# Kernel tuning notes

Hardware: AMD Instinct MI355X
Metric: run time of the kernel (lower is better)

## Reference

```python
import jax, jax.numpy as jnp
import numpy as np

N = 20000        # atoms
NEIGH = 12       # neighbors per atom
BSTEPS = 40      # bond GBF steps, range [0, 8]
ASTEPS = 20      # angle GBF steps, range [-1, 1]
H = 64           # hidden size
NCLS = 2         # n_classification
NCRYS = 20       # crystals (contiguous blocks of 1000 atoms)
NREL = 3         # edge relation types


def gbf(data, dmin, dmax, steps):
    # Gaussian basis expansion: exp(-(d - mu)^2 / gamma^2), gamma = (max-min)/steps
    filters = jnp.linspace(dmin, dmax, steps)
    gamma = (dmax - dmin) / steps
    return jnp.exp(-((data[..., None] - filters) ** 2) / gamma ** 2)


def rgcn(x, src, dst, etype, W_rel, W_root, b):
    # RGCNConv (PyG default): out = x @ W_root + b + sum_r mean_{j in N_r(i)} x_j @ W_r
    out = x @ W_root + b
    for r in range(NREL):
        w = (etype == r).astype(x.dtype)                     # [E]
        msg = (x @ W_rel[r])[src] * w[:, None]               # transform-then-gather: [E, H]
        s = jax.ops.segment_sum(msg, dst, num_segments=x.shape[0])
        c = jax.ops.segment_sum(w, dst, num_segments=x.shape[0])
        out = out + s / jnp.maximum(c, 1.0)[:, None]
    return out


def _forward(bond_fea, angle_fea, species, nbr_idx, crys_idx,
             W1b_rel, W1b_root, b1b, W1a_rel, W1a_root, b1a,
             W2b_rel, W2b_root, b2b, W2a_rel, W2a_root, b2a,
             fc_W, fc_b):
    n = bond_fea.shape[0]
    src = jnp.repeat(jnp.arange(n, dtype=jnp.int32), NEIGH)  # edge sources
    dst = nbr_idx.reshape(-1)                                # edge targets
    etype = species[src] + species[dst]                      # 0/1/2 per species pair

    edge_fea = gbf(bond_fea, 0.0, 8.0, BSTEPS).reshape(n, -1)      # [N, 480]
    ang_fea = gbf(angle_fea, -1.0, 1.0, ASTEPS).reshape(n, -1)     # [N, 2880]

    bf = jax.nn.relu(rgcn(edge_fea, src, dst, etype, W1b_rel, W1b_root, b1b))
    af = jax.nn.relu(rgcn(ang_fea, src, dst, etype, W1a_rel, W1a_root, b1a))
    # dropout treated as identity (eval/deterministic reference)
    bf = jax.nn.relu(rgcn(bf, src, dst, etype, W2b_rel, W2b_root, b2b))
    af = jax.nn.relu(rgcn(af, src, dst, etype, W2a_rel, W2a_root, b2a))

    feat = jnp.concatenate([bf, af], axis=1)                 # [N, 128]

    # pool: mean over contiguous [start, end) ranges per crystal
    starts = crys_idx[:, 0]
    crys_id = jnp.searchsorted(starts, jnp.arange(n), side='right') - 1
    sums = jax.ops.segment_sum(feat, crys_id, num_segments=NCRYS)
    counts = (crys_idx[:, 1] - crys_idx[:, 0]).astype(feat.dtype)[:, None]
    pooled = sums / counts                                   # [NCRYS, 128]

    return pooled @ fc_W + fc_b                              # [NCRYS, NCLS]


def setup_inputs() -> dict:
    key = jax.random.key(0)
    ks = jax.random.split(key, 20)
    bond_fea = jax.random.uniform(ks[0], (N, NEIGH), dtype=jnp.float32) * 8.0
    angle_fea = jax.random.uniform(ks[1], (N, NEIGH, NEIGH), dtype=jnp.float32) * 2.0 - 1.0
    species = jax.random.randint(ks[2], (N,), 0, 2, dtype=jnp.int32)
    nbr_idx = jax.random.randint(ks[3], (N, NEIGH), 0, N, dtype=jnp.int32)
    starts = jnp.arange(NCRYS, dtype=jnp.int32) * (N // NCRYS)
    crys_idx = jnp.stack([starts, starts + (N // NCRYS)], axis=1)

    def w(k, shape, fan_in):
        return jax.random.normal(k, shape, dtype=jnp.float32) / np.sqrt(fan_in)

    in_b = BSTEPS * NEIGH            # 480
    in_a = ASTEPS * NEIGH * NEIGH    # 2880
    return {
        'bond_fea': bond_fea, 'angle_fea': angle_fea, 'species': species,
        'nbr_idx': nbr_idx, 'crys_idx': crys_idx,
        'W1b_rel': w(ks[4], (NREL, in_b, H), in_b), 'W1b_root': w(ks[5], (in_b, H), in_b),
        'b1b': jnp.zeros((H,), jnp.float32),
        'W1a_rel': w(ks[6], (NREL, in_a, H), in_a), 'W1a_root': w(ks[7], (in_a, H), in_a),
        'b1a': jnp.zeros((H,), jnp.float32),
        'W2b_rel': w(ks[8], (NREL, H, H), H), 'W2b_root': w(ks[9], (H, H), H),
        'b2b': jnp.zeros((H,), jnp.float32),
        'W2a_rel': w(ks[10], (NREL, H, H), H), 'W2a_root': w(ks[11], (H, H), H),
        'b2a': jnp.zeros((H,), jnp.float32),
        'fc_W': w(ks[12], (2 * H, NCLS), 2 * H), 'fc_b': jnp.zeros((NCLS,), jnp.float32),
    }


def reference(bond_fea, angle_fea, species, nbr_idx, crys_idx,
              W1b_rel, W1b_root, b1b, W1a_rel, W1a_root, b1a,
              W2b_rel, W2b_root, b2b, W2a_rel, W2a_root, b2a,
              fc_W, fc_b):
    return _forward(bond_fea, angle_fea, species, nbr_idx, crys_idx,
                    W1b_rel, W1b_root, b1b, W1a_rel, W1a_root, b1a,
                    W2b_rel, W2b_root, b2b, W2a_rel, W2a_root, b2a,
                    fc_W, fc_b)
```

## Files before the change

kernel.cpp:

```cpp
#include <hip/hip_runtime.h>

#define NN 20000
#define NNP 20096
#define NEIGH 12
#define NCRYS 20
#define MT2 1256
#define NSUB 16

typedef __bf16 bf16x8 __attribute__((ext_vector_type(8)));
typedef __bf16 bf16x4 __attribute__((ext_vector_type(4)));
typedef float f32x4 __attribute__((ext_vector_type(4)));

__device__ __forceinline__ void pack_one(const float* Wrel, const float* Wroot,
                                         __bf16* Wp, int K, int idx) {
    int k = idx >> 8, n = idx & 255;
    int r = n >> 6, h = n & 63;
    float v = (r < 3) ? Wrel[((size_t)r * K + k) * 64 + h] : Wroot[(size_t)k * 64 + h];
    int kt = k >> 5, k8 = (k >> 3) & 3, j = k & 7, nt = n >> 4, ni = n & 15;
    Wp[((((size_t)kt * 16 + nt) * 4 + k8) * 16 + ni) * 8 + j] = (__bf16)v;
}

__global__ __launch_bounds__(256) void setup_kernel(
    const int* __restrict__ species, const int* __restrict__ nbr,
    int* __restrict__ adj, int* __restrict__ deg,
    const float* __restrict__ W1b_rel, const float* __restrict__ W1b_root,
    const float* __restrict__ W1a_rel, const float* __restrict__ W1a_root,
    const float* __restrict__ W2b_rel, const float* __restrict__ W2b_root,
    const float* __restrict__ W2a_rel, const float* __restrict__ W2a_root,
    __bf16* __restrict__ Wp1b, __bf16* __restrict__ Wp1a,
    __bf16* __restrict__ Wp2b, __bf16* __restrict__ Wp2a,
    const float* __restrict__ bond, const float* __restrict__ angle,
    float* __restrict__ bondT, float* __restrict__ angleT) {
    __shared__ float ls[64 * 145];
    const int bx = blockIdx.x, tid = threadIdx.x;
    if (bx < 938) {
        int e = bx * 256 + tid;
        if (e < NN * NEIGH) {
            int i = e / NEIGH;
            int d = nbr[e];
            int r = species[i] + species[d];
            int slot = atomicAdd(&deg[d], 1);
            if (slot < 64) adj[(size_t)d * 64 + slot] = i | (r << 28);
        }
    } else if (bx < 938 + 256) {
        const int S0 = 480 * 256, S1 = S0 + 2880 * 256, S2 = S1 + 64 * 256, S3 = S2 + 64 * 256;
        for (int idx = (bx - 938) * 256 + tid; idx < S3; idx += 256 * 256) {
            if (idx < S0)       pack_one(W1b_rel, W1b_root, Wp1b, 480, idx);
            else if (idx < S1)  pack_one(W1a_rel, W1a_root, Wp1a, 2880, idx - S0);
            else if (idx < S2)  pack_one(W2b_rel, W2b_root, Wp2b, 64, idx - S1);
            else                pack_one(W2a_rel, W2a_root, Wp2a, 64, idx - S2);
        }
    } else {
        int tb = bx - 1194;
        if (tb < 314) {
            int m0 = tb * 64;
            for (int idx = tid; idx < 64 * 144; idx += 256) {
                int mm = idx / 144, j = idx - mm * 144;
                int m = m0 + mm;
                ls[mm * 145 + j] = (m < NN) ? angle[(size_t)m * 144 + j] : 0.f;
            }
            __syncthreads();
            for (int idx = tid; idx < 144 * 64; idx += 256) {
                int j = idx >> 6, mm = idx & 63;
                angleT[(size_t)j * NNP + m0 + mm] = ls[mm * 145 + j];
            }
        } else {
            int m0 = (tb - 314) * 64;
            for (int idx = tid; idx < 64 * 12; idx += 256) {
                int mm = idx / 12, j = idx - mm * 12;
                int m = m0 + mm;
                ls[mm * 13 + j] = (m < NN) ? bond[(size_t)m * 12 + j] : 0.f;
            }
            __syncthreads();
            for (int idx = tid; idx < 12 * 64; idx += 256) {
                int j = idx >> 6, mm = idx & 63;
                bondT[(size_t)j * NNP + m0 + mm] = ls[mm * 13 + j];
            }
        }
    }
}

template <int MODE>
__device__ __forceinline__ void gemm1_body(const float* __restrict__ xT,
                                           const __bf16* __restrict__ Wp,
                                           float* __restrict__ Y, int mb,
                                           __bf16* __restrict__ Al) {
    constexpr int KTOT = (MODE == 0) ? 480 : 2880;
    constexpr int NKT = KTOT / 32;
    constexpr int DIVN = (MODE == 0) ? 40 : 20;
    constexpr float F0 = (MODE == 0) ? 0.f : -1.f;
    constexpr float FS = (MODE == 0) ? (8.f / 39.f) : (2.f / 19.f);
    constexpr float NG2 = ((MODE == 0) ? -25.f : -100.f) * 1.44269504f;
    const float C  = __builtin_amdgcn_exp2f(2.f * NG2 * FS * FS);
    const float P1 = NG2 * FS * FS;
    const float P2 = -2.f * NG2 * FS;

    const int tid = threadIdx.x;
    const int lane = tid & 63, wv = tid >> 6;
    const int m0 = mb * 64;
    const int smt = tid >> 7;
    const int sk8 = (tid >> 5) & 3;
    const int smi = (tid >> 1) & 15;
    const int sjh = (tid & 1) * 4;
    const int sgm = m0 + smt * 16 + smi;
    const int kk0 = sk8 * 8 + sjh;
    const int swoff = (((smt * 4 + sk8) * 16 + smi) * 8 + sjh);
    const int k8b = lane >> 4, nib = lane & 15;
    const bf16x8* Bg = (const bf16x8*)Wp;

    f32x4 acc[4][2] = {};
    bf16x8 bcur[2], bnx[2], bnx2[2];

    auto bload = [&](int kt, bf16x8* d) {
#pragma unroll
        for (int jf = 0; jf < 2; ++jf)
            d[jf] = Bg[(((size_t)kt * 16 + 2 * wv + jf) * 4 + k8b) * 16 + nib];
    };
    auto aload = [&](int kt) -> float {
        int k = kt * 32 + kk0;
        int jr = k / DIVN;
        return xT[(size_t)jr * NNP + sgm];
    };
    auto stage = [&](int kt, float a, __bf16* dst) {
        int k = kt * 32 + kk0;
        int jr = k / DIVN;
        int s = k - jr * DIVN;
        float d0 = a - (F0 + (float)s * FS);
        float e0 = __builtin_amdgcn_exp2f(NG2 * d0 * d0);
        float q0 = __builtin_amdgcn_exp2f(fmaf(P2, d0, P1));
        float e1 = e0 * q0;
        float q1 = q0 * C;
        float e2 = e1 * q1;
        float e3 = e2 * q1 * C;
        bf16x4 vals;
        vals[0] = (__bf16)e0; vals[1] = (__bf16)e1;
        vals[2] = (__bf16)e2; vals[3] = (__bf16)e3;
        *(bf16x4*)&dst[swoff] = vals;
    };

    {
        float a0 = aload(0);
        stage(0, a0, Al);
    }
    float anext = aload(1 < NKT ? 1 : 0);
    bload(0, bcur);
    bload(1 < NKT ? 1 : 0, bnx);
    __syncthreads();

    for (int kt = 0; kt < NKT; ++kt) {
        __bf16* Ab = Al + ((kt & 1) << 11);
        __bf16* An = Al + (((kt & 1) ^ 1) << 11);
        const int ktp2 = (kt + 2 < NKT) ? kt + 2 : NKT - 1;
        bload(ktp2, bnx2);
        float afut = (kt + 2 < NKT) ? aload(kt + 2) : anext;
        bf16x8 af[4];
#pragma unroll
        for (int t = 0; t < 4; ++t)
            af[t] = *(const bf16x8*)&Ab[((((t << 2) + k8b) << 4) + nib) << 3];
#pragma unroll
        for (int i = 0; i < 4; ++i)
#pragma unroll
            for (int j = 0; j < 2; ++j)
                acc[i][j] = __builtin_amdgcn_mfma_f32_16x16x32_bf16(af[i], bcur[j], acc[i][j], 0, 0, 0);
        if (kt + 1 < NKT)
            stage(kt + 1, anext, An);
        __syncthreads();
#pragma unroll
        for (int j = 0; j < 2; ++j) { bcur[j] = bnx[j]; bnx[j] = bnx2[j]; }
        anext = afut;
    }

    const int mrow0 = m0 + ((lane >> 4) << 2);
    const int ncol = (wv << 5) + nib;
#pragma unroll
    for (int i = 0; i < 4; ++i)
#pragma unroll
        for (int j = 0; j < 2; ++j)
#pragma unroll
            for (int v = 0; v < 4; ++v) {
                int m = mrow0 + i * 16 + v;
                if (m < NN) Y[(size_t)m * 256 + ncol + j * 16] = acc[i][j][v];
            }
}

__global__ __launch_bounds__(512, 4) void mega_gemm1(const float* __restrict__ bondT,
                                                     const float* __restrict__ angleT,
                                                     const __bf16* __restrict__ Wp1b,
                                                     const __bf16* __restrict__ Wp1a,
                                                     float* __restrict__ Yb, float* __restrict__ Ya) {
    __shared__ __align__(16) __bf16 Al[2 * 2048];
    int bx = blockIdx.x;
    if (bx < 314) gemm1_body<1>(angleT, Wp1a, Ya, bx, Al);
    else          gemm1_body<0>(bondT, Wp1b, Yb, bx - 314, Al);
}

__global__ __launch_bounds__(256) void mega_gemm2(const __bf16* __restrict__ Hbp,
                                                  const __bf16* __restrict__ Hap,
                                                  const __bf16* __restrict__ Wp2b,
                                                  const __bf16* __restrict__ Wp2a,
                                                  float* __restrict__ Yb, float* __restrict__ Ya) {
    __shared__ __align__(16) __bf16 Al[4096];
    __shared__ __align__(16) __bf16 Bl[4096];
    const int ch = blockIdx.x & 1;
    const int mb = blockIdx.x >> 1;
    const int nb = blockIdx.y;
    const __bf16* Ap = ch ? Hap : Hbp;
    const __bf16* Wp = ch ? Wp2a : Wp2b;
    float* Y = ch ? Ya : Yb;
    const int tid = threadIdx.x;
    const int lane = tid & 63, wv = tid >> 6;
    const int m0 = mb * 128;
    const int rw = wv & 1, cw = wv >> 1;
    f32x4 acc[4][4] = {};
#pragma unroll
    for (int kt = 0; kt < 2; ++kt) {
        __syncthreads();
        {
            const float4* src = (const float4*)(Wp + (((size_t)kt * 16 + nb * 8) << 9));
            float4* dst = (float4*)Bl;
            float4 v0 = src[tid], v1 = src[tid + 256];
            dst[tid] = v0;
            dst[tid + 256] = v1;
        }
        {
            const float4* src = (const float4*)(Ap + (((size_t)kt * MT2 + mb * 8) << 9));
            float4* dst = (float4*)Al;
            float4 v0 = src[tid], v1 = src[tid + 256];
            dst[tid] = v0;
            dst[tid + 256] = v1;
        }
        __syncthreads();
        bf16x8 af[4], bfr[4];
        int fro = ((lane >> 4) << 4) + (lane & 15);
#pragma unroll
        for (int t4 = 0; t4 < 4; ++t4) {
            af[t4] = *(const bf16x8*)&Al[((((rw * 4 + t4) << 6) + fro) << 3)];
            bfr[t4] = *(const bf16x8*)&Bl[((((cw * 4 + t4) << 6) + fro) << 3)];
        }
#pragma unroll
        for (int i = 0; i < 4; ++i)
#pragma unroll
            for (int j = 0; j < 4; ++j)
                acc[i][j] = __builtin_amdgcn_mfma_f32_16x16x32_bf16(af[i], bfr[j], acc[i][j], 0, 0, 0);
    }
    const int n0 = nb * 128 + cw * 64;
    const int mrow0 = m0 + rw * 64 + ((lane >> 4) << 2);
    const int ncol = n0 + (lane & 15);
#pragma unroll
    for (int i = 0; i < 4; ++i)
#pragma unroll
        for (int j = 0; j < 4; ++j)
#pragma unroll
            for (int v = 0; v < 4; ++v) {
                int m = mrow0 + i * 16 + v;
                if (m < NN) Y[(size_t)m * 256 + ncol + j * 16] = acc[i][j][v];
            }
}

__device__ __forceinline__ float agg_node(const float* __restrict__ Y,
                                          const int* __restrict__ adj,
                                          const int* __restrict__ deg,
                                          const float* __restrict__ bias,
                                          int node, int h) {
    int dg = min(deg[node], 64);
    int e = adj[(size_t)node * 64 + h];
    bool val = h < dg;
    int r = e >> 28;
    unsigned long long bl0 = __ballot(val && r == 0);
    unsigned long long bl1 = __ballot(val && r == 1);
    unsigned long long bl2 = __ballot(val && r == 2);
    int c0 = __popcll(bl0), c1 = __popcll(bl1), c2 = __popcll(bl2);
    float s0 = 0.f, s1 = 0.f, s2 = 0.f;
    if (dg > 0) {
        int e0 = __builtin_amdgcn_readfirstlane(e);
        int ec = val ? e : e0;
        for (int k0 = 0; k0 < dg; k0 += 16) {
            float v[16];
#pragma unroll
            for (int i = 0; i < 16; ++i) {
                int ek = __builtin_amdgcn_readlane(ec, k0 + i);
                v[i] = Y[(size_t)(ek & 0x0FFFFFFF) * 256 + (ek >> 28) * 64 + h];
            }
#pragma unroll
            for (int i = 0; i < 16; ++i) {
                int kk = k0 + i;
                if (kk < dg) {
                    int rr = __builtin_amdgcn_readlane(ec, kk) >> 28;
                    if (rr == 0) s0 += v[i];
                    else if (rr == 1) s1 += v[i];
                    else s2 += v[i];
                }
            }
        }
    }
    float o = Y[(size_t)node * 256 + 192 + h] + bias[h] +
              s0 / fmaxf((float)c0, 1.f) + s1 / fmaxf((float)c1, 1.f) +
              s2 / fmaxf((float)c2, 1.f);
    return fmaxf(o, 0.f);
}

__global__ __launch_bounds__(256) void agg_packed(const float* __restrict__ Yb,
                                                  const float* __restrict__ Ya,
                                                  const int* __restrict__ adj,
                                                  const int* __restrict__ deg,
                                                  const float* __restrict__ biasb,
                                                  const float* __restrict__ biasa,
                                                  __bf16* __restrict__ outb,
                                                  __bf16* __restrict__ outa) {
    const float* Y = blockIdx.y ? Ya : Yb;
    const float* bias = blockIdx.y ? biasa : biasb;
    __bf16* outp = blockIdx.y ? outa : outb;
    int node = blockIdx.x * 4 + (threadIdx.x >> 6);
    int h = threadIdx.x & 63;
    float o = (node < NN) ? agg_node(Y, adj, deg, bias, node, h) : 0.f;
    int mt = node >> 4, mi = node & 15;
    int ktt = h >> 5, k8 = (h >> 3) & 3, j = h & 7;
    outp[((((size_t)ktt * MT2 + mt) * 4 + k8) * 16 + mi) * 8 + j] = (__bf16)o;
}

__global__ __launch_bounds__(256) void agg_pool(const float* __restrict__ Yb,
                                                const float* __restrict__ Ya,
                                                const int* __restrict__ adj,
                                                const int* __restrict__ deg,
                                                const float* __restrict__ biasb,
                                                const float* __restrict__ biasa,
                                                const int* __restrict__ crys,
                                                float* __restrict__ pooled) {
    const float* Y = blockIdx.y ? Ya : Yb;
    const float* bias = blockIdx.y ? biasa : biasb;
    const int base = blockIdx.y ? 64 : 0;
    int node = blockIdx.x * 4 + (threadIdx.x >> 6);
    int h = threadIdx.x & 63;
    if (node >= NN) return;
    float o = agg_node(Y, adj, deg, bias, node, h);
    int c = 0;
#pragma unroll
    for (int t = 1; t < NCRYS; ++t) c += (node >= crys[t * 2]) ? 1 : 0;
    int sub = blockIdx.x & (NSUB - 1);
    atomicAdd(&pooled[((size_t)c * NSUB + sub) * 128 + base + h], o);
}

__global__ void final2(const float* __restrict__ pooled, const int* __restrict__ crys,
                       const float* __restrict__ fcW, const float* __restrict__ fcb,
                       float* __restrict__ out) {
    int c = blockIdx.x >> 1, o = blockIdx.x & 1;
    int l = threadIdx.x;
    float cnt = (float)(crys[c * 2 + 1] - crys[c * 2]);
    float sb = 0.f, sa = 0.f;
    for (int s = 0; s < NSUB; ++s) {
        sb += pooled[((size_t)c * NSUB + s) * 128 + l];
        sa += pooled[((size_t)c * NSUB + s) * 128 + 64 + l];
    }
    float a = sb * fcW[l * 2 + o] + sa * fcW[(64 + l) * 2 + o];
    for (int s = 32; s > 0; s >>= 1) a += __shfl_down(a, s);
    if (l == 0) out[c * 2 + o] = a / cnt + fcb[o];
}

extern "C" void kernel_launch(void* const* d_in, const int* in_sizes, int n_in,
                              void* d_out, int out_size, void* d_ws, size_t ws_size,
                              hipStream_t stream) {
    const float* bond    = (const float*)d_in[0];
    const float* angle   = (const float*)d_in[1];
    const int*   species = (const int*)d_in[2];
    const int*   nbr     = (const int*)d_in[3];
    const int*   crys    = (const int*)d_in[4];
    const float* W1b_rel = (const float*)d_in[5];
    const float* W1b_root= (const float*)d_in[6];
    const float* b1b     = (const float*)d_in[7];
    const float* W1a_rel = (const float*)d_in[8];
    const float* W1a_root= (const float*)d_in[9];
    const float* b1a     = (const float*)d_in[10];
    const float* W2b_rel = (const float*)d_in[11];
    const float* W2b_root= (const float*)d_in[12];
    const float* b2b     = (const float*)d_in[13];
    const float* W2a_rel = (const float*)d_in[14];
    const float* W2a_root= (const float*)d_in[15];
    const float* b2a     = (const float*)d_in[16];
    const float* fcW     = (const float*)d_in[17];
    const float* fcb     = (const float*)d_in[18];
    float* out = (float*)d_out;

    char* ws = (char*)d_ws;
    size_t off = 0;
    auto alloc = [&](size_t bytes) {
        char* p = ws + off;
        off = (off + bytes + 255) & ~(size_t)255;
        return p;
    };
    __bf16* Wp1b = (__bf16*)alloc((size_t)480 * 256 * 2);
    __bf16* Wp1a = (__bf16*)alloc((size_t)2880 * 256 * 2);
    __bf16* Wp2b = (__bf16*)alloc((size_t)64 * 256 * 2);
    __bf16* Wp2a = (__bf16*)alloc((size_t)64 * 256 * 2);
    float*  bondT = (float*)alloc((size_t)12 * NNP * 4);
    float*  angleT= (float*)alloc((size_t)144 * NNP * 4);
    float*  Yb   = (float*)alloc((size_t)NN * 256 * 4);
    float*  Ya   = (float*)alloc((size_t)NN * 256 * 4);
    __bf16* Hbp  = (__bf16*)alloc((size_t)2 * MT2 * 512 * 2);
    __bf16* Hap  = (__bf16*)alloc((size_t)2 * MT2 * 512 * 2);
    int*    adj  = (int*)alloc((size_t)NN * 64 * 4);
    int*    deg  = (int*)alloc((size_t)NN * 4);
    float*  pooled = (float*)alloc((size_t)NCRYS * NSUB * 128 * 4);

    hipMemsetAsync(deg, 0, (size_t)NN * 4, stream);
    hipMemsetAsync(pooled, 0, (size_t)NCRYS * NSUB * 128 * 4, stream);

    setup_kernel<<<1822, 256, 0, stream>>>(species, nbr, adj, deg,
                                           W1b_rel, W1b_root, W1a_rel, W1a_root,
                                           W2b_rel, W2b_root, W2a_rel, W2a_root,
                                           Wp1b, Wp1a, Wp2b, Wp2a,
                                           bond, angle, bondT, angleT);

    mega_gemm1<<<628, 512, 0, stream>>>(bondT, angleT, Wp1b, Wp1a, Yb, Ya);
    agg_packed<<<dim3(5024, 2), 256, 0, stream>>>(Yb, Ya, adj, deg, b1b, b1a, Hbp, Hap);
    mega_gemm2<<<dim3(314, 2), 256, 0, stream>>>(Hbp, Hap, Wp2b, Wp2a, Yb, Ya);
    agg_pool<<<dim3(5000, 2), 256, 0, stream>>>(Yb, Ya, adj, deg, b2b, b2a, crys, pooled);
    final2<<<NCRYS * 2, 64, 0, stream>>>(pooled, crys, fcW, fcb, out);
}
```

Measured before the change: 256.9 us.

## Process two K-tiles per barrier in first-layer GEMM and interleave bond/angle blocks

The first-layer fused GBF+GEMM now stages two 32-wide K tiles per iteration into a doubled LDS buffer, so it needs half as many barriers. The bond weights are zero-padded from K=480 to 512 and an extra zero row is added to the transposed bond input so the tile count is even. The GBF index and row offset are now advanced incrementally instead of being recomputed with integer divides, and bond and angle blocks are interleaved by even/odd block index to balance load across the grid. In exchange it uses more LDS and registers per block and does a little padded MFMA work on the bond path.

Result: slower. 281.9 us (+9.7%).

```diff
diff --git a/kernel.cpp b/kernel.cpp
--- a/kernel.cpp
+++ b/kernel.cpp
@@ -12,10 +12,12 @@
 typedef float f32x4 __attribute__((ext_vector_type(4)));
 
 __device__ __forceinline__ void pack_one(const float* Wrel, const float* Wroot,
-                                         __bf16* Wp, int K, int idx) {
+                                         __bf16* Wp, int K, int KV, int idx) {
     int k = idx >> 8, n = idx & 255;
     int r = n >> 6, h = n & 63;
-    float v = (r < 3) ? Wrel[((size_t)r * K + k) * 64 + h] : Wroot[(size_t)k * 64 + h];
+    float v = 0.f;
+    if (k < KV)
+        v = (r < 3) ? Wrel[((size_t)r * KV + k) * 64 + h] : Wroot[(size_t)k * 64 + h];
     int kt = k >> 5, k8 = (k >> 3) & 3, j = k & 7, nt = n >> 4, ni = n & 15;
     Wp[((((size_t)kt * 16 + nt) * 4 + k8) * 16 + ni) * 8 + j] = (__bf16)v;
 }
@@ -43,12 +45,12 @@
             if (slot < 64) adj[(size_t)d * 64 + slot] = i | (r << 28);
         }
     } else if (bx < 938 + 256) {
-        const int S0 = 480 * 256, S1 = S0 + 2880 * 256, S2 = S1 + 64 * 256, S3 = S2 + 64 * 256;
+        const int S0 = 512 * 256, S1 = S0 + 2880 * 256, S2 = S1 + 64 * 256, S3 = S2 + 64 * 256;
         for (int idx = (bx - 938) * 256 + tid; idx < S3; idx += 256 * 256) {
-            if (idx < S0)       pack_one(W1b_rel, W1b_root, Wp1b, 480, idx);
-            else if (idx < S1)  pack_one(W1a_rel, W1a_root, Wp1a, 2880, idx - S0);
-            else if (idx < S2)  pack_one(W2b_rel, W2b_root, Wp2b, 64, idx - S1);
-            else                pack_one(W2a_rel, W2a_root, Wp2a, 64, idx - S2);
+            if (idx < S0)       pack_one(W1b_rel, W1b_root, Wp1b, 512, 480, idx);
+            else if (idx < S1)  pack_one(W1a_rel, W1a_root, Wp1a, 2880, 2880, idx - S0);
+            else if (idx < S2)  pack_one(W2b_rel, W2b_root, Wp2b, 64, 64, idx - S1);
+            else                pack_one(W2a_rel, W2a_root, Wp2a, 64, 64, idx - S2);
         }
     } else {
         int tb = bx - 1194;
@@ -72,9 +74,9 @@
                 ls[mm * 13 + j] = (m < NN) ? bond[(size_t)m * 12 + j] : 0.f;
             }
             __syncthreads();
-            for (int idx = tid; idx < 12 * 64; idx += 256) {
+            for (int idx = tid; idx < 13 * 64; idx += 256) {
                 int j = idx >> 6, mm = idx & 63;
-                bondT[(size_t)j * NNP + m0 + mm] = ls[mm * 13 + j];
+                bondT[(size_t)j * NNP + m0 + mm] = (j < 12) ? ls[mm * 13 + j] : 0.f;
             }
         }
     }
@@ -85,9 +87,10 @@
                                            const __bf16* __restrict__ Wp,
                                            float* __restrict__ Y, int mb,
                                            __bf16* __restrict__ Al) {
-    constexpr int KTOT = (MODE == 0) ? 480 : 2880;
-    constexpr int NKT = KTOT / 32;
+    constexpr int NKT2 = (MODE == 0) ? 8 : 45;
     constexpr int DIVN = (MODE == 0) ? 40 : 20;
+    constexpr int DS   = (MODE == 0) ? 24 : 4;
+    constexpr int DJR  = (MODE == 0) ? 1 : 3;
     constexpr float F0 = (MODE == 0) ? 0.f : -1.f;
     constexpr float FS = (MODE == 0) ? (8.f / 39.f) : (2.f / 19.f);
     constexpr float NG2 = ((MODE == 0) ? -25.f : -100.f) * 1.44269504f;
@@ -98,76 +101,92 @@
     const int tid = threadIdx.x;
     const int lane = tid & 63, wv = tid >> 6;
     const int m0 = mb * 64;
-    const int smt = tid >> 7;
-    const int sk8 = (tid >> 5) & 3;
-    const int smi = (tid >> 1) & 15;
-    const int sjh = (tid & 1) * 4;
+    const int smt = tid >> 7, sk8 = (tid >> 5) & 3;
+    const int smi = (tid >> 1) & 15, sjh = (tid & 1) * 4;
     const int sgm = m0 + smt * 16 + smi;
     const int kk0 = sk8 * 8 + sjh;
-    const int swoff = (((smt * 4 + sk8) * 16 + smi) * 8 + sjh);
+    const int swoff = ((smt * 4 + sk8) * 16 + smi) * 8 + sjh;
     const int k8b = lane >> 4, nib = lane & 15;
     const bf16x8* Bg = (const bf16x8*)Wp;
 
+    int s0 = kk0 % DIVN, s1 = (kk0 + 32) % DIVN;
+    int off0 = (kk0 / DIVN) * NNP + sgm;
+    int off1 = ((kk0 + 32) / DIVN) * NNP + sgm;
+    int bidx = ((wv * 2) * 4 + k8b) * 16 + nib;
+
     f32x4 acc[4][2] = {};
-    bf16x8 bcur[2], bnx[2], bnx2[2];
-
-    auto bload = [&](int kt, bf16x8* d) {
-#pragma unroll
-        for (int jf = 0; jf < 2; ++jf)
-            d[jf] = Bg[(((size_t)kt * 16 + 2 * wv + jf) * 4 + k8b) * 16 + nib];
-    };
-    auto aload = [&](int kt) -> float {
-        int k = kt * 32 + kk0;
-        int jr = k / DIVN;
-        return xT[(size_t)jr * NNP + sgm];
-    };
-    auto stage = [&](int kt, float a, __bf16* dst) {
-        int k = kt * 32 + kk0;
-        int jr = k / DIVN;
-        int s = k - jr * DIVN;
-        float d0 = a - (F0 + (float)s * FS);
+    bf16x8 bcur[4], bnx[4];
+
+    auto gbf4s = [&](float a, int s) -> bf16x4 {
+        float f = fmaf((float)s, FS, F0);
+        float d0 = a - f;
         float e0 = __builtin_amdgcn_exp2f(NG2 * d0 * d0);
         float q0 = __builtin_amdgcn_exp2f(fmaf(P2, d0, P1));
         float e1 = e0 * q0;
         float q1 = q0 * C;
         float e2 = e1 * q1;
         float e3 = e2 * q1 * C;
-        bf16x4 vals;
-        vals[0] = (__bf16)e0; vals[1] = (__bf16)e1;
-        vals[2] = (__bf16)e2; vals[3] = (__bf16)e3;
-        *(bf16x4*)&dst[swoff] = vals;
+        bf16x4 v;
+        v[0] = (__bf16)e0; v[1] = (__bf16)e1; v[2] = (__bf16)e2; v[3] = (__bf16)e3;
+        return v;
     };
+    auto adv = [&]() {
+        s0 += DS; off0 += DJR * NNP; if (s0 >= DIVN) { s0 -= DIVN; off0 += NNP; }
+        s1 += DS; off1 += DJR * NNP; if (s1 >= DIVN) { s1 -= DIVN; off1 += NNP; }
+    };
 
     {
-        float a0 = aload(0);
-        stage(0, a0, Al);
-    }
-    float anext = aload(1 < NKT ? 1 : 0);
-    bload(0, bcur);
-    bload(1 < NKT ? 1 : 0, bnx);
+        float a0 = xT[off0], a1 = xT[off1];
+#pragma unroll
+        for (int sub = 0; sub < 2; ++sub)
+#pragma unroll
+            for (int jf = 0; jf < 2; ++jf)
+                bcur[sub * 2 + jf] = Bg[bidx + sub * 1024 + jf * 64];
+        *(bf16x4*)&Al[swoff] = gbf4s(a0, s0);
+        *(bf16x4*)&Al[2048 + swoff] = gbf4s(a1, s1);
+        adv();
+        bidx += 2048;
+    }
     __syncthreads();
 
-    for (int kt = 0; kt < NKT; ++kt) {
-        __bf16* Ab = Al + ((kt & 1) << 11);
-        __bf16* An = Al + (((kt & 1) ^ 1) << 11);
-        const int ktp2 = (kt + 2 < NKT) ? kt + 2 : NKT - 1;
-        bload(ktp2, bnx2);
-        float afut = (kt + 2 < NKT) ? aload(kt + 2) : anext;
-        bf16x8 af[4];
-#pragma unroll
-        for (int t = 0; t < 4; ++t)
-            af[t] = *(const bf16x8*)&Ab[((((t << 2) + k8b) << 4) + nib) << 3];
-#pragma unroll
-        for (int i = 0; i < 4; ++i)
-#pragma unroll
-            for (int j = 0; j < 2; ++j)
-                acc[i][j] = __builtin_amdgcn_mfma_f32_16x16x32_bf16(af[i], bcur[j], acc[i][j], 0, 0, 0);
-        if (kt + 1 < NKT)
-            stage(kt + 1, anext, An);
+    for (int kt = 0; kt < NKT2; ++kt) {
+        __bf16* Ab = Al + ((kt & 1) << 12);
+        __bf16* An = Al + (((kt & 1) ^ 1) << 12);
+        const bool more = (kt + 1 < NKT2);
+        float an0, an1;
+        int cs0 = s0, cs1 = s1;
+        if (more) {
+            an0 = xT[off0];
+            an1 = xT[off1];
+#pragma unroll
+            for (int sub = 0; sub < 2; ++sub)
+#pragma unroll
+                for (int jf = 0; jf < 2; ++jf)
+                    bnx[sub * 2 + jf] = Bg[bidx + sub * 1024 + jf * 64];
+            adv();
+            bidx += 2048;
+        }
+#pragma unroll
+        for (int sub = 0; sub < 2; ++sub) {
+            bf16x8 af[4];
+#pragma unroll
+            for (int t = 0; t < 4; ++t)
+                af[t] = *(const bf16x8*)&Ab[(sub << 11) + ((((t << 2) + k8b) << 4) + nib) * 8];
+#pragma unroll
+            for (int i = 0; i < 4; ++i)
+#pragma unroll
+                for (int j = 0; j < 2; ++j)
+                    acc[i][j] = __builtin_amdgcn_mfma_f32_16x16x32_bf16(af[i], bcur[sub * 2 + j], acc[i][j], 0, 0, 0);
+        }
+        if (more) {
+            *(bf16x4*)&An[swoff] = gbf4s(an0, cs0);
+            *(bf16x4*)&An[2048 + swoff] = gbf4s(an1, cs1);
+        }
         __syncthreads();
-#pragma unroll
-        for (int j = 0; j < 2; ++j) { bcur[j] = bnx[j]; bnx[j] = bnx2[j]; }
-        anext = afut;
+        if (more) {
+#pragma unroll
+            for (int q = 0; q < 4; ++q) bcur[q] = bnx[q];
+        }
     }
 
     const int mrow0 = m0 + ((lane >> 4) << 2);
@@ -188,10 +207,10 @@
                                                      const __bf16* __restrict__ Wp1b,
                                                      const __bf16* __restrict__ Wp1a,
                                                      float* __restrict__ Yb, float* __restrict__ Ya) {
-    __shared__ __align__(16) __bf16 Al[2 * 2048];
+    __shared__ __align__(16) __bf16 Al[2 * 4096];
     int bx = blockIdx.x;
-    if (bx < 314) gemm1_body<1>(angleT, Wp1a, Ya, bx, Al);
-    else          gemm1_body<0>(bondT, Wp1b, Yb, bx - 314, Al);
+    if ((bx & 1) == 0) gemm1_body<1>(angleT, Wp1a, Ya, bx >> 1, Al);
+    else               gemm1_body<0>(bondT, Wp1b, Yb, bx >> 1, Al);
 }
 
 __global__ __launch_bounds__(256) void mega_gemm2(const __bf16* __restrict__ Hbp,
@@ -387,11 +406,11 @@
         off = (off + bytes + 255) & ~(size_t)255;
         return p;
     };
-    __bf16* Wp1b = (__bf16*)alloc((size_t)480 * 256 * 2);
+    __bf16* Wp1b = (__bf16*)alloc((size_t)512 * 256 * 2);
     __bf16* Wp1a = (__bf16*)alloc((size_t)2880 * 256 * 2);
     __bf16* Wp2b = (__bf16*)alloc((size_t)64 * 256 * 2);
     __bf16* Wp2a = (__bf16*)alloc((size_t)64 * 256 * 2);
-    float*  bondT = (float*)alloc((size_t)12 * NNP * 4);
+    float*  bondT = (float*)alloc((size_t)13 * NNP * 4);
     float*  angleT= (float*)alloc((size_t)144 * NNP * 4);
     float*  Yb   = (float*)alloc((size_t)NN * 256 * 4);
     float*  Ya   = (float*)alloc((size_t)NN * 256 * 4);
```
